# Kernel optimization log

Measured on AMD Instinct MI355X. Metric: run time of the kernel, lower is better.

The kernel has to match this reference:

```python
import jax, jax.numpy as jnp
import numpy as np

TEMPERATURE = 0.1
B, D, A = 8192, 256, 4


def setup_inputs() -> dict:
    key = jax.random.key(0)
    k1, k2 = jax.random.split(key)
    # scale by 1/sqrt(D) so dot products are O(1) and exp(sim/T) is finite
    embeddings = jax.random.normal(k1, (B, D), dtype=jnp.float32) / jnp.sqrt(jnp.float32(D))
    labels = jax.random.randint(k2, (B, A), 0, 6, dtype=jnp.int64)
    return {"embeddings": embeddings, "labels": labels}


def reference(embeddings, labels):
    b = embeddings.shape[0]
    # [B, B] similarity scaled by temperature
    sim = jnp.matmul(embeddings, embeddings.T) / TEMPERATURE
    # positive mask: ANY aspect matches (vectorized over aspects), diagonal zeroed
    pos_mask = jnp.any(labels[:, None, :] == labels[None, :, :], axis=-1)
    pos_mask = pos_mask & ~jnp.eye(b, dtype=bool)
    pos_mask = pos_mask.astype(sim.dtype)

    exp_sim = jnp.exp(sim)
    positive_sim = jnp.sum(exp_sim * pos_mask, axis=1)            # [B]
    all_sim = jnp.sum(exp_sim, axis=1) - jnp.diagonal(exp_sim)   # [B]

    valid = positive_sim > 0
    pos_safe = jnp.where(valid, positive_sim, 1.0)
    all_safe = jnp.where(valid, all_sim, 1.0)
    row_loss = jnp.where(valid, -jnp.log(pos_safe / (all_safe + 1e-8)), 0.0)

    num_pos = jnp.sum(valid.astype(sim.dtype))
    loss = jnp.where(num_pos > 0, jnp.sum(row_loss) / jnp.maximum(num_pos, 1.0), 0.0)
    return loss
```

## Files before the change

kernel.cpp:

```cpp
#include <hip/hip_runtime.h>
#include <stdint.h>

typedef short short8 __attribute__((ext_vector_type(8)));
typedef float f32x4 __attribute__((ext_vector_type(4)));
typedef float f32x2 __attribute__((ext_vector_type(2)));

#define B_TOTAL 8192
#define DDIM 256
#define BM 128
#define BN 64
#define NSPLIT 16
#define COLS_PER (B_TOTAL / NSPLIT)
#define ITERS (COLS_PER / BN)
#define NBLOCKS ((B_TOTAL / BM) * NSPLIT)
#define SCALE_HALF 3.79828546f
#define LN2F 0.6931471805599453f

typedef __attribute__((address_space(3))) char lds_char;
typedef __attribute__((address_space(1))) const char gbl_char;

__device__ __forceinline__ unsigned short f2bf(float f) {
  unsigned int u = __builtin_bit_cast(unsigned int, f);
  u = (u + 0x7FFFu + ((u >> 16) & 1u)) >> 16;
  return (unsigned short)u;
}

__global__ __launch_bounds__(256) void prep_all(
    const float* __restrict__ E, const int* __restrict__ lab,
    unsigned short* __restrict__ Eb, unsigned int* __restrict__ plab,
    float* __restrict__ posAll) {
  const int t = blockIdx.x * 256 + threadIdx.x;
  const float4* s4 = (const float4*)E + (size_t)t * 2;
  float4 v0 = s4[0], v1 = s4[1];
  short8 o;
  o[0] = (short)f2bf(v0.x * SCALE_HALF); o[1] = (short)f2bf(v0.y * SCALE_HALF);
  o[2] = (short)f2bf(v0.z * SCALE_HALF); o[3] = (short)f2bf(v0.w * SCALE_HALF);
  o[4] = (short)f2bf(v1.x * SCALE_HALF); o[5] = (short)f2bf(v1.y * SCALE_HALF);
  o[6] = (short)f2bf(v1.z * SCALE_HALF); o[7] = (short)f2bf(v1.w * SCALE_HALF);
  *(short8*)(Eb + (size_t)t * 8) = o;
  if (t < B_TOTAL) {
    int4 l = ((const int4*)lab)[t];
    plab[t] = (1u << ((unsigned)l.x & 31u))
            | (1u << (((unsigned)l.y & 31u) + 6u))
            | (1u << (((unsigned)l.z & 31u) + 12u))
            | (1u << (((unsigned)l.w & 31u) + 18u));
  }
  if (t < 2 * B_TOTAL) posAll[t] = 0.0f;
}

struct __align__(16) SMem {
  char btile[BN * DDIM * 2];
  unsigned int plds[BN];
};

template <int DIAG>
__device__ __forceinline__ void do_epilogue(
    const f32x4 (&acc)[4][2], int colbase, int l15,
    const unsigned int (&pi)[2][4], const int (&irow)[2][4],
    const unsigned int* plds, f32x2 (&pos2)[2][2], f32x2 (&all2)[2][2]) {
#pragma unroll
  for (int n = 0; n < 4; ++n) {
    const int j = colbase + n * 16 + l15;
    const unsigned int hj = plds[n * 16 + l15];
#pragma unroll
    for (int m = 0; m < 2; ++m) {
      float e[4];
#pragma unroll
      for (int q = 0; q < 4; ++q) {
        float v = __builtin_amdgcn_exp2f(acc[n][m][q]);
        if (DIAG) { if (j == irow[m][q]) v = 0.0f; }
        e[q] = v;
      }
      f32x2 p01 = { (pi[m][0] & hj) ? e[0] : 0.0f, (pi[m][1] & hj) ? e[1] : 0.0f };
      f32x2 p23 = { (pi[m][2] & hj) ? e[2] : 0.0f, (pi[m][3] & hj) ? e[3] : 0.0f };
      all2[m][0] += (f32x2){e[0], e[1]};
      all2[m][1] += (f32x2){e[2], e[3]};
      pos2[m][0] += p01;
      pos2[m][1] += p23;
    }
  }
}

__global__ __launch_bounds__(256, 2) void main_kernel(
    const unsigned short* __restrict__ Eb, const unsigned int* __restrict__ plab,
    float* __restrict__ posArr, float* __restrict__ allArr) {
  __shared__ SMem sm;
  const int tid = threadIdx.x;
  const int lane = tid & 63;
  const int wid = tid >> 6;
  const int l15 = lane & 15;
  const int l4 = lane >> 4;
  const int rb = (int)blockIdx.x & 63;
  const int cs = (int)blockIdx.x >> 6;
  const int rowbase = rb * BM;
  const int colstart = cs * COLS_PER;

  short8 afrag[2][8];
#pragma unroll
  for (int m = 0; m < 2; ++m) {
    const int row = rowbase + wid * 32 + m * 16 + l15;
    const unsigned short* rp = Eb + (size_t)row * DDIM + l4 * 8;
#pragma unroll
    for (int k = 0; k < 8; ++k) afrag[m][k] = *(const short8*)(rp + k * 32);
  }

  unsigned int pi[2][4];
  int irow[2][4];
#pragma unroll
  for (int m = 0; m < 2; ++m)
#pragma unroll
    for (int q = 0; q < 4; ++q) {
      const int i = rowbase + wid * 32 + m * 16 + l4 * 4 + q;
      irow[m][q] = i;
      pi[m][q] = plab[i];
    }

  f32x2 pos2[2][2] = {};
  f32x2 all2[2][2] = {};

  for (int it = 0; it < ITERS; ++it) {
    const int colbase = colstart + it * BN;
    __syncthreads();
#pragma unroll
    for (int q = 0; q < 8; ++q) {
      const unsigned int L = (unsigned int)wid * 8192u + (unsigned int)q * 1024u +
                             (unsigned int)lane * 16u;
      const unsigned int r = L >> 9;
      const unsigned int s = (L >> 4) & 31u;
      const unsigned int c = s ^ (r & 7u);
      const char* src = (const char*)(Eb + (size_t)(colbase + (int)r) * DDIM + c * 8);
      char* dst = sm.btile + (unsigned int)wid * 8192u + (unsigned int)q * 1024u;
      __builtin_amdgcn_global_load_lds((gbl_char*)src, (lds_char*)dst, 16, 0, 0);
    }
    if (tid < BN) sm.plds[tid] = plab[colbase + tid];
    __syncthreads();

    f32x4 acc[4][2];
#pragma unroll
    for (int n = 0; n < 4; ++n)
#pragma unroll
      for (int m = 0; m < 2; ++m) acc[n][m] = (f32x4){0.f, 0.f, 0.f, 0.f};

#pragma unroll
    for (int k = 0; k < 8; ++k) {
      short8 b[4];
#pragma unroll
      for (int n = 0; n < 4; ++n) {
        const unsigned int rr = (unsigned int)(n * 16 + l15);
        const unsigned int cdx = (unsigned int)(k * 4 + l4);
        const unsigned int s = cdx ^ (rr & 7u);
        b[n] = *(const short8*)(sm.btile + rr * 512u + s * 16u);
      }
#pragma unroll
      for (int n = 0; n < 4; ++n)
#pragma unroll
        for (int m = 0; m < 2; ++m)
          acc[n][m] = __builtin_amdgcn_mfma_f32_16x16x32_bf16(
              afrag[m][k], b[n], acc[n][m], 0, 0, 0);
    }

    const bool hasDiag = (colbase < rowbase + BM) && (rowbase < colbase + BN);
    if (hasDiag)
      do_epilogue<1>(acc, colbase, l15, pi, irow, sm.plds, pos2, all2);
    else
      do_epilogue<0>(acc, colbase, l15, pi, irow, sm.plds, pos2, all2);
  }

#pragma unroll
  for (int m = 0; m < 2; ++m)
#pragma unroll
    for (int q = 0; q < 4; ++q) {
      float p = pos2[m][q >> 1][q & 1], al = all2[m][q >> 1][q & 1];
      p += __shfl_xor(p, 1); p += __shfl_xor(p, 2);
      p += __shfl_xor(p, 4); p += __shfl_xor(p, 8);
      al += __shfl_xor(al, 1); al += __shfl_xor(al, 2);
      al += __shfl_xor(al, 4); al += __shfl_xor(al, 8);
      if (l15 == 0) {
        atomicAdd(&posArr[irow[m][q]], p);
        atomicAdd(&allArr[irow[m][q]], al);
      }
    }
}

__global__ __launch_bounds__(1024) void finalize_kernel(
    const float* __restrict__ posArr, const float* __restrict__ allArr,
    float* __restrict__ out) {
  float ls = 0.f, cnt = 0.f;
#pragma unroll
  for (int k = 0; k < B_TOTAL / 1024; ++k) {
    const int i = threadIdx.x + (k << 10);
    const float p = posArr[i];
    const float a = allArr[i];
    if (p > 0.f) {
      ls += (__builtin_amdgcn_logf(a + 1e-8f) - __builtin_amdgcn_logf(p)) * LN2F;
      cnt += 1.f;
    }
  }
#pragma unroll
  for (int msk = 1; msk < 64; msk <<= 1) {
    ls += __shfl_xor(ls, msk);
    cnt += __shfl_xor(cnt, msk);
  }
  __shared__ float sls[16], scnt[16];
  const int w = threadIdx.x >> 6;
  if ((threadIdx.x & 63) == 0) { sls[w] = ls; scnt[w] = cnt; }
  __syncthreads();
  if (threadIdx.x == 0) {
    float L = 0.f, C = 0.f;
    for (int i = 0; i < 16; ++i) { L += sls[i]; C += scnt[i]; }
    out[0] = (C > 0.f) ? L / fmaxf(C, 1.f) : 0.f;
  }
}

extern "C" void kernel_launch(void* const* d_in, const int* in_sizes, int n_in,
                              void* d_out, int out_size, void* d_ws, size_t ws_size,
                              hipStream_t stream) {
  const float* E = (const float*)d_in[0];
  const int* lab = (const int*)d_in[1];
  float* out = (float*)d_out;
  char* ws = (char*)d_ws;

  unsigned short* Eb = (unsigned short*)ws;
  unsigned int* plab = (unsigned int*)(ws + 4u * 1024u * 1024u);
  float* posArr = (float*)(ws + 4u * 1024u * 1024u + 32u * 1024u);
  float* allArr = posArr + B_TOTAL;

  prep_all<<<1024, 256, 0, stream>>>(E, lab, Eb, plab, posArr);
  main_kernel<<<NBLOCKS, 256, 0, stream>>>(Eb, plab, posArr, allArr);
  finalize_kernel<<<1, 1024, 0, stream>>>(posArr, allArr, out);
}
```

Before: 110.7 us.

## Double-buffer B tiles with async LDS prefetch and preload column labels

Halves the column tile width and adds a second LDS buffer so the next tile's global-to-LDS loads are issued before computing on the current one. Ordering relies on explicit vmcnt waits and raw s_barrier in place of __syncthreads. All column labels for the block's range are loaded into LDS once up front, so the per-iteration label fetch goes away. The aim is to hide global load latency behind MFMA and exp work. In exchange there are twice as many iterations and barriers, and less MFMA work per barrier. Correctness depends on the hand-written waitcnt values matching the async-copy semantics.

```diff
diff --git a/kernel.cpp b/kernel.cpp
--- a/kernel.cpp
+++ b/kernel.cpp
@@ -8,7 +8,7 @@
 #define B_TOTAL 8192
 #define DDIM 256
 #define BM 128
-#define BN 64
+#define BN 32
 #define NSPLIT 16
 #define COLS_PER (B_TOTAL / NSPLIT)
 #define ITERS (COLS_PER / BN)
@@ -49,19 +49,19 @@
 }
 
 struct __align__(16) SMem {
-  char btile[BN * DDIM * 2];
-  unsigned int plds[BN];
+  char btile[2][BN * DDIM * 2];
+  unsigned int plab_all[COLS_PER];
 };
 
 template <int DIAG>
 __device__ __forceinline__ void do_epilogue(
-    const f32x4 (&acc)[4][2], int colbase, int l15,
+    const f32x4 (&acc)[2][2], int colbase, int it, int l15,
     const unsigned int (&pi)[2][4], const int (&irow)[2][4],
-    const unsigned int* plds, f32x2 (&pos2)[2][2], f32x2 (&all2)[2][2]) {
-#pragma unroll
-  for (int n = 0; n < 4; ++n) {
+    const unsigned int* plab_all, f32x2 (&pos2)[2][2], f32x2 (&all2)[2][2]) {
+#pragma unroll
+  for (int n = 0; n < 2; ++n) {
     const int j = colbase + n * 16 + l15;
-    const unsigned int hj = plds[n * 16 + l15];
+    const unsigned int hj = plab_all[it * BN + n * 16 + l15];
 #pragma unroll
     for (int m = 0; m < 2; ++m) {
       float e[4];
@@ -95,6 +95,20 @@
   const int rowbase = rb * BM;
   const int colstart = cs * COLS_PER;
 
+  auto stage = [&](int bufi, int cb) {
+#pragma unroll
+    for (int q = 0; q < 4; ++q) {
+      const unsigned int L = (unsigned int)wid * 4096u + (unsigned int)q * 1024u +
+                             (unsigned int)lane * 16u;
+      const unsigned int r = L >> 9;
+      const unsigned int s = (L >> 4) & 31u;
+      const unsigned int c = s ^ (r & 7u);
+      const char* src = (const char*)(Eb + (size_t)(cb + (int)r) * DDIM + c * 8);
+      char* dst = sm.btile[bufi] + (unsigned int)wid * 4096u + (unsigned int)q * 1024u;
+      __builtin_amdgcn_global_load_lds((gbl_char*)src, (lds_char*)dst, 16, 0, 0);
+    }
+  };
+
   short8 afrag[2][8];
 #pragma unroll
   for (int m = 0; m < 2; ++m) {
@@ -102,6 +116,13 @@
     const unsigned short* rp = Eb + (size_t)row * DDIM + l4 * 8;
 #pragma unroll
     for (int k = 0; k < 8; ++k) afrag[m][k] = *(const short8*)(rp + k * 32);
+  }
+
+  {
+    unsigned int a0 = plab[colstart + tid];
+    unsigned int a1 = plab[colstart + 256 + tid];
+    sm.plab_all[tid] = a0;
+    sm.plab_all[tid + 256] = a1;
   }
 
   unsigned int pi[2][4];
@@ -115,44 +136,44 @@
       pi[m][q] = plab[i];
     }
 
+  stage(0, colstart);
+  asm volatile("s_waitcnt lgkmcnt(0)" ::: "memory");
+  __builtin_amdgcn_sched_barrier(0);
+
   f32x2 pos2[2][2] = {};
   f32x2 all2[2][2] = {};
 
   for (int it = 0; it < ITERS; ++it) {
     const int colbase = colstart + it * BN;
-    __syncthreads();
-#pragma unroll
-    for (int q = 0; q < 8; ++q) {
-      const unsigned int L = (unsigned int)wid * 8192u + (unsigned int)q * 1024u +
-                             (unsigned int)lane * 16u;
-      const unsigned int r = L >> 9;
-      const unsigned int s = (L >> 4) & 31u;
-      const unsigned int c = s ^ (r & 7u);
-      const char* src = (const char*)(Eb + (size_t)(colbase + (int)r) * DDIM + c * 8);
-      char* dst = sm.btile + (unsigned int)wid * 8192u + (unsigned int)q * 1024u;
-      __builtin_amdgcn_global_load_lds((gbl_char*)src, (lds_char*)dst, 16, 0, 0);
-    }
-    if (tid < BN) sm.plds[tid] = plab[colbase + tid];
-    __syncthreads();
-
-    f32x4 acc[4][2];
-#pragma unroll
-    for (int n = 0; n < 4; ++n)
+    const int cur = it & 1;
+
+    if (it + 1 < ITERS) {
+      stage(cur ^ 1, colbase + BN);
+      asm volatile("s_waitcnt vmcnt(4)" ::: "memory");
+    } else {
+      asm volatile("s_waitcnt vmcnt(0)" ::: "memory");
+    }
+    __builtin_amdgcn_s_barrier();
+    __builtin_amdgcn_sched_barrier(0);
+
+    f32x4 acc[2][2];
+#pragma unroll
+    for (int n = 0; n < 2; ++n)
 #pragma unroll
       for (int m = 0; m < 2; ++m) acc[n][m] = (f32x4){0.f, 0.f, 0.f, 0.f};
 
 #pragma unroll
     for (int k = 0; k < 8; ++k) {
-      short8 b[4];
-#pragma unroll
-      for (int n = 0; n < 4; ++n) {
+      short8 b[2];
+#pragma unroll
+      for (int n = 0; n < 2; ++n) {
         const unsigned int rr = (unsigned int)(n * 16 + l15);
         const unsigned int cdx = (unsigned int)(k * 4 + l4);
         const unsigned int s = cdx ^ (rr & 7u);
-        b[n] = *(const short8*)(sm.btile + rr * 512u + s * 16u);
+        b[n] = *(const short8*)(sm.btile[cur] + rr * 512u + s * 16u);
       }
 #pragma unroll
-      for (int n = 0; n < 4; ++n)
+      for (int n = 0; n < 2; ++n)
 #pragma unroll
         for (int m = 0; m < 2; ++m)
           acc[n][m] = __builtin_amdgcn_mfma_f32_16x16x32_bf16(
@@ -161,9 +182,12 @@
 
     const bool hasDiag = (colbase < rowbase + BM) && (rowbase < colbase + BN);
     if (hasDiag)
-      do_epilogue<1>(acc, colbase, l15, pi, irow, sm.plds, pos2, all2);
+      do_epilogue<1>(acc, colbase, it, l15, pi, irow, sm.plab_all, pos2, all2);
     else
-      do_epilogue<0>(acc, colbase, l15, pi, irow, sm.plds, pos2, all2);
+      do_epilogue<0>(acc, colbase, it, l15, pi, irow, sm.plab_all, pos2, all2);
+
+    __builtin_amdgcn_s_barrier();
+    __builtin_amdgcn_sched_barrier(0);
   }
 
 #pragma unroll
```

Measured after the change: 108.9 us. Within noise of the previous version (-1.6%).

## Exploit symmetry of similarity matrix: compute upper-triangular tile pairs only

Applied to the files above, without the earlier changes.

Since the similarity matrix and the any-match mask are both symmetric, the kernel now computes only the upper-triangular 128x128 tile pairs, listed in a lookup table built by the prep kernel. Each off-diagonal tile adds its row sums and also its column sums, using extra cross-lane shuffles and atomics on the column indices, so the MFMA and exp work is roughly halved. Each block now handles one tile with a single LDS load and no inner loop, and MFMA priority is raised with s_setprio. The cost is more atomic traffic, a larger LDS footprint that may lower occupancy, and 2080 short-lived blocks where there used to be fewer looping blocks.

```diff
diff --git a/kernel.cpp b/kernel.cpp
--- a/kernel.cpp
+++ b/kernel.cpp
@@ -7,12 +7,9 @@
 
 #define B_TOTAL 8192
 #define DDIM 256
-#define BM 128
-#define BN 64
-#define NSPLIT 16
-#define COLS_PER (B_TOTAL / NSPLIT)
-#define ITERS (COLS_PER / BN)
-#define NBLOCKS ((B_TOTAL / BM) * NSPLIT)
+#define TILE 128
+#define NTILE (B_TOTAL / TILE)
+#define NPAIRS (NTILE * (NTILE + 1) / 2)
 #define SCALE_HALF 3.79828546f
 #define LN2F 0.6931471805599453f
 
@@ -28,7 +25,7 @@
 __global__ __launch_bounds__(256) void prep_all(
     const float* __restrict__ E, const int* __restrict__ lab,
     unsigned short* __restrict__ Eb, unsigned int* __restrict__ plab,
-    float* __restrict__ posAll) {
+    float* __restrict__ posAll, unsigned int* __restrict__ lut) {
   const int t = blockIdx.x * 256 + threadIdx.x;
   const float4* s4 = (const float4*)E + (size_t)t * 2;
   float4 v0 = s4[0], v1 = s4[1];
@@ -46,43 +43,98 @@
             | (1u << (((unsigned)l.w & 31u) + 18u));
   }
   if (t < 2 * B_TOTAL) posAll[t] = 0.0f;
+  if (t < NTILE * NTILE) {
+    const int I = t >> 6, J = t & 63;
+    if (J >= I) {
+      const int idx = I * NTILE - (I * (I - 1)) / 2 + (J - I);
+      lut[idx] = ((unsigned)I << 8) | (unsigned)J;
+    }
+  }
 }
 
 struct __align__(16) SMem {
-  char btile[BN * DDIM * 2];
-  unsigned int plds[BN];
+  char btile[TILE * DDIM * 2];
+  unsigned int plab_col[TILE];
 };
 
 template <int DIAG>
-__device__ __forceinline__ void do_epilogue(
-    const f32x4 (&acc)[4][2], int colbase, int l15,
-    const unsigned int (&pi)[2][4], const int (&irow)[2][4],
-    const unsigned int* plds, f32x2 (&pos2)[2][2], f32x2 (&all2)[2][2]) {
-#pragma unroll
-  for (int n = 0; n < 4; ++n) {
-    const int j = colbase + n * 16 + l15;
-    const unsigned int hj = plds[n * 16 + l15];
-#pragma unroll
-    for (int m = 0; m < 2; ++m) {
-      float e[4];
-#pragma unroll
-      for (int q = 0; q < 4; ++q) {
-        float v = __builtin_amdgcn_exp2f(acc[n][m][q]);
-        if (DIAG) { if (j == irow[m][q]) v = 0.0f; }
-        e[q] = v;
-      }
-      f32x2 p01 = { (pi[m][0] & hj) ? e[0] : 0.0f, (pi[m][1] & hj) ? e[1] : 0.0f };
-      f32x2 p23 = { (pi[m][2] & hj) ? e[2] : 0.0f, (pi[m][3] & hj) ? e[3] : 0.0f };
-      all2[m][0] += (f32x2){e[0], e[1]};
-      all2[m][1] += (f32x2){e[2], e[3]};
-      pos2[m][0] += p01;
-      pos2[m][1] += p23;
+__device__ __forceinline__ void compute_tile(
+    const char* btile, const unsigned int* plab_col,
+    const short8 (&afrag)[2][8], const unsigned int (&pi)[2][4],
+    int l15, int l4, int wid, int colbase,
+    float* posArr, float* allArr,
+    f32x2 (&pos2)[2][2], f32x2 (&all2)[2][2]) {
+#pragma unroll
+  for (int nq = 0; nq < 4; ++nq) {
+    f32x4 acc[2][2];
+#pragma unroll
+    for (int n2 = 0; n2 < 2; ++n2)
+#pragma unroll
+      for (int m = 0; m < 2; ++m) acc[n2][m] = (f32x4){0.f, 0.f, 0.f, 0.f};
+
+    __builtin_amdgcn_s_setprio(1);
+#pragma unroll
+    for (int k = 0; k < 8; ++k) {
+      short8 b[2];
+#pragma unroll
+      for (int n2 = 0; n2 < 2; ++n2) {
+        const unsigned int rr = (unsigned int)(nq * 32 + n2 * 16 + l15);
+        const unsigned int s = (unsigned int)(k * 4 + l4) ^ (rr & 7u);
+        b[n2] = *(const short8*)(btile + rr * 512u + s * 16u);
+      }
+#pragma unroll
+      for (int n2 = 0; n2 < 2; ++n2)
+#pragma unroll
+        for (int m = 0; m < 2; ++m)
+          acc[n2][m] = __builtin_amdgcn_mfma_f32_16x16x32_bf16(
+              afrag[m][k], b[n2], acc[n2][m], 0, 0, 0);
+    }
+    __builtin_amdgcn_s_setprio(0);
+
+    float colp[2] = {0.f, 0.f}, cola[2] = {0.f, 0.f};
+#pragma unroll
+    for (int n2 = 0; n2 < 2; ++n2) {
+      const int jloc = nq * 32 + n2 * 16 + l15;
+      const unsigned int hj = plab_col[jloc];
+#pragma unroll
+      for (int m = 0; m < 2; ++m) {
+        float e[4];
+#pragma unroll
+        for (int q = 0; q < 4; ++q) {
+          float v = __builtin_amdgcn_exp2f(acc[n2][m][q]);
+          if (DIAG) { if (jloc == wid * 32 + m * 16 + l4 * 4 + q) v = 0.0f; }
+          e[q] = v;
+        }
+        f32x2 p01 = { (pi[m][0] & hj) ? e[0] : 0.f, (pi[m][1] & hj) ? e[1] : 0.f };
+        f32x2 p23 = { (pi[m][2] & hj) ? e[2] : 0.f, (pi[m][3] & hj) ? e[3] : 0.f };
+        all2[m][0] += (f32x2){e[0], e[1]};
+        all2[m][1] += (f32x2){e[2], e[3]};
+        pos2[m][0] += p01;
+        pos2[m][1] += p23;
+        if (!DIAG) {
+          cola[n2] += (e[0] + e[1]) + (e[2] + e[3]);
+          colp[n2] += (p01[0] + p01[1]) + (p23[0] + p23[1]);
+        }
+      }
+    }
+    if (!DIAG) {
+#pragma unroll
+      for (int n2 = 0; n2 < 2; ++n2) {
+        float cp = colp[n2], ca = cola[n2];
+        cp += __shfl_xor(cp, 16); cp += __shfl_xor(cp, 32);
+        ca += __shfl_xor(ca, 16); ca += __shfl_xor(ca, 32);
+        if (l4 == 0) {
+          atomicAdd(&posArr[colbase + nq * 32 + n2 * 16 + l15], cp);
+          atomicAdd(&allArr[colbase + nq * 32 + n2 * 16 + l15], ca);
+        }
+      }
     }
   }
 }
 
 __global__ __launch_bounds__(256, 2) void main_kernel(
     const unsigned short* __restrict__ Eb, const unsigned int* __restrict__ plab,
+    const unsigned int* __restrict__ lut,
     float* __restrict__ posArr, float* __restrict__ allArr) {
   __shared__ SMem sm;
   const int tid = threadIdx.x;
@@ -90,10 +142,23 @@
   const int wid = tid >> 6;
   const int l15 = lane & 15;
   const int l4 = lane >> 4;
-  const int rb = (int)blockIdx.x & 63;
-  const int cs = (int)blockIdx.x >> 6;
-  const int rowbase = rb * BM;
-  const int colstart = cs * COLS_PER;
+  const unsigned int pair = lut[blockIdx.x];
+  const int I = (int)(pair >> 8), J = (int)(pair & 255u);
+  const int rowbase = I * TILE;
+  const int colbase = J * TILE;
+  const int row0 = rowbase + wid * 32 + l4 * 4;
+
+#pragma unroll
+  for (int q = 0; q < 16; ++q) {
+    const unsigned int L = (unsigned int)wid * 16384u + (unsigned int)q * 1024u +
+                           (unsigned int)lane * 16u;
+    const unsigned int r = L >> 9;
+    const unsigned int s = (L >> 4) & 31u;
+    const unsigned int c = s ^ (r & 7u);
+    const char* src = (const char*)(Eb + (size_t)(colbase + (int)r) * DDIM + c * 8);
+    char* dst = sm.btile + (unsigned int)wid * 16384u + (unsigned int)q * 1024u;
+    __builtin_amdgcn_global_load_lds((gbl_char*)src, (lds_char*)dst, 16, 0, 0);
+  }
 
   short8 afrag[2][8];
 #pragma unroll
@@ -104,67 +169,27 @@
     for (int k = 0; k < 8; ++k) afrag[m][k] = *(const short8*)(rp + k * 32);
   }
 
+  if (tid < TILE) sm.plab_col[tid] = plab[colbase + tid];
+
   unsigned int pi[2][4];
-  int irow[2][4];
 #pragma unroll
   for (int m = 0; m < 2; ++m)
 #pragma unroll
-    for (int q = 0; q < 4; ++q) {
-      const int i = rowbase + wid * 32 + m * 16 + l4 * 4 + q;
-      irow[m][q] = i;
-      pi[m][q] = plab[i];
-    }
+    for (int q = 0; q < 4; ++q) pi[m][q] = plab[row0 + m * 16 + q];
+
+  asm volatile("s_waitcnt vmcnt(0) lgkmcnt(0)" ::: "memory");
+  __builtin_amdgcn_s_barrier();
+  __builtin_amdgcn_sched_barrier(0);
 
   f32x2 pos2[2][2] = {};
   f32x2 all2[2][2] = {};
 
-  for (int it = 0; it < ITERS; ++it) {
-    const int colbase = colstart + it * BN;
-    __syncthreads();
-#pragma unroll
-    for (int q = 0; q < 8; ++q) {
-      const unsigned int L = (unsigned int)wid * 8192u + (unsigned int)q * 1024u +
-                             (unsigned int)lane * 16u;
-      const unsigned int r = L >> 9;
-      const unsigned int s = (L >> 4) & 31u;
-      const unsigned int c = s ^ (r & 7u);
-      const char* src = (const char*)(Eb + (size_t)(colbase + (int)r) * DDIM + c * 8);
-      char* dst = sm.btile + (unsigned int)wid * 8192u + (unsigned int)q * 1024u;
-      __builtin_amdgcn_global_load_lds((gbl_char*)src, (lds_char*)dst, 16, 0, 0);
-    }
-    if (tid < BN) sm.plds[tid] = plab[colbase + tid];
-    __syncthreads();
-
-    f32x4 acc[4][2];
-#pragma unroll
-    for (int n = 0; n < 4; ++n)
-#pragma unroll
-      for (int m = 0; m < 2; ++m) acc[n][m] = (f32x4){0.f, 0.f, 0.f, 0.f};
-
-#pragma unroll
-    for (int k = 0; k < 8; ++k) {
-      short8 b[4];
-#pragma unroll
-      for (int n = 0; n < 4; ++n) {
-        const unsigned int rr = (unsigned int)(n * 16 + l15);
-        const unsigned int cdx = (unsigned int)(k * 4 + l4);
-        const unsigned int s = cdx ^ (rr & 7u);
-        b[n] = *(const short8*)(sm.btile + rr * 512u + s * 16u);
-      }
-#pragma unroll
-      for (int n = 0; n < 4; ++n)
-#pragma unroll
-        for (int m = 0; m < 2; ++m)
-          acc[n][m] = __builtin_amdgcn_mfma_f32_16x16x32_bf16(
-              afrag[m][k], b[n], acc[n][m], 0, 0, 0);
-    }
-
-    const bool hasDiag = (colbase < rowbase + BM) && (rowbase < colbase + BN);
-    if (hasDiag)
-      do_epilogue<1>(acc, colbase, l15, pi, irow, sm.plds, pos2, all2);
-    else
-      do_epilogue<0>(acc, colbase, l15, pi, irow, sm.plds, pos2, all2);
-  }
+  if (I == J)
+    compute_tile<1>(sm.btile, sm.plab_col, afrag, pi, l15, l4, wid, colbase,
+                    posArr, allArr, pos2, all2);
+  else
+    compute_tile<0>(sm.btile, sm.plab_col, afrag, pi, l15, l4, wid, colbase,
+                    posArr, allArr, pos2, all2);
 
 #pragma unroll
   for (int m = 0; m < 2; ++m)
@@ -176,8 +201,8 @@
       al += __shfl_xor(al, 1); al += __shfl_xor(al, 2);
       al += __shfl_xor(al, 4); al += __shfl_xor(al, 8);
       if (l15 == 0) {
-        atomicAdd(&posArr[irow[m][q]], p);
-        atomicAdd(&allArr[irow[m][q]], al);
+        atomicAdd(&posArr[row0 + m * 16 + q], p);
+        atomicAdd(&allArr[row0 + m * 16 + q], al);
       }
     }
 }
@@ -224,8 +249,9 @@
   unsigned int* plab = (unsigned int*)(ws + 4u * 1024u * 1024u);
   float* posArr = (float*)(ws + 4u * 1024u * 1024u + 32u * 1024u);
   float* allArr = posArr + B_TOTAL;
-
-  prep_all<<<1024, 256, 0, stream>>>(E, lab, Eb, plab, posArr);
-  main_kernel<<<NBLOCKS, 256, 0, stream>>>(Eb, plab, posArr, allArr);
+  unsigned int* lut = (unsigned int*)(allArr + B_TOTAL);
+
+  prep_all<<<1024, 256, 0, stream>>>(E, lab, Eb, plab, posArr, lut);
+  main_kernel<<<NPAIRS, 256, 0, stream>>>(Eb, plab, lut, posArr, allArr);
   finalize_kernel<<<1, 1024, 0, stream>>>(posArr, allArr, out);
 }
```

Result: slower. 126.3 us (+14.1%).
